# Kernel optimization log

Measured on AMD Instinct MI355X. Metric: run time of the kernel, lower is better.

The kernel has to match this reference:

```python
import jax, jax.numpy as jnp
import numpy as np

HIDDEN = 128


def setup_inputs() -> dict:
    key = jax.random.key(0)
    ks = jax.random.split(key, 9)
    N, D, OUT, DIM = 200000, 128, 128, 10000
    msg = jax.random.normal(ks[0], (N, D), dtype=jnp.float32)
    t = jax.random.uniform(ks[1], (N,), dtype=jnp.float32)
    index = jax.random.randint(ks[2], (N,), 0, DIM, dtype=jnp.int32)
    s = 1.0 / np.sqrt(HIDDEN)
    uni = lambda k, shape: jax.random.uniform(k, shape, jnp.float32, -s, s)
    return {
        "msg": msg,
        "t": t,
        "index": index,
        "dim_size": DIM,
        "W_ih": uni(ks[3], (3 * HIDDEN, D)),
        "W_hh": uni(ks[4], (3 * HIDDEN, HIDDEN)),
        "b_ih": uni(ks[5], (3 * HIDDEN,)),
        "b_hh": uni(ks[6], (3 * HIDDEN,)),
        "W_mlp": uni(ks[7], (OUT, HIDDEN)),
        "b_mlp": uni(ks[8], (OUT,)),
    }


def reference(msg, t, index, dim_size, W_ih, W_hh, b_ih, b_hh, W_mlp, b_mlp):
    # Sort messages by node id (primary) and timestamp (secondary). This matches
    # torch: sort by t, then group by index preserving time order within group.
    H = W_hh.shape[1]
    order = jnp.lexsort((t, index))
    idx_s = index[order]          # [N]
    msg_s = msg[order]            # [N, D]
    # segment starts: hidden state resets to 0 at the first message of each node
    start = jnp.concatenate([jnp.ones((1,), bool), idx_s[1:] != idx_s[:-1]])
    # precompute input-gate projections for all messages at once: [N, 3H]
    gi = msg_s @ W_ih.T + b_ih

    def step(h, inp):
        gi_t, st = inp
        h0 = jnp.where(st, jnp.zeros_like(h), h)
        gh = h0 @ W_hh.T + b_hh
        i_r, i_z, i_n = jnp.split(gi_t, 3)
        h_r, h_z, h_n = jnp.split(gh, 3)
        r = jax.nn.sigmoid(i_r + h_r)
        z = jax.nn.sigmoid(i_z + h_z)
        n = jnp.tanh(i_n + r * h_n)
        hn = (1.0 - z) * n + z * h0
        return hn, hn

    h0 = jnp.zeros((H,), msg.dtype)
    _, h_all = jax.lax.scan(step, h0, (gi, start))  # [N, H]

    # final hidden per node = hidden at last (latest-timestamp) message of that node
    pos = jnp.arange(idx_s.shape[0], dtype=jnp.int32)
    last_pos = jax.ops.segment_max(pos, idx_s, num_segments=dim_size)  # empty -> int32 min
    has_msg = last_pos >= 0
    h_node = h_all[jnp.clip(last_pos, 0, None)]     # [dim_size, H]
    out_vals = h_node @ W_mlp.T + b_mlp             # [dim_size, OUT]
    return jnp.where(has_msg[:, None], out_vals, jnp.zeros_like(out_vals))
```

## Files before the change

### kernel.cpp

```cpp
#include <hip/hip_runtime.h>
#include <hip/hip_fp16.h>

typedef _Float16 f16;
typedef _Float16 f16x8 __attribute__((ext_vector_type(8)));
typedef _Float16 f16x4 __attribute__((ext_vector_type(4)));
typedef float    f32x4 __attribute__((ext_vector_type(4)));
typedef unsigned long long u64;
typedef unsigned int u32;

#define HIDDEN 128
#define G3     384

__device__ inline float sigm(float x) { return 1.f / (1.f + __expf(-x)); }
__device__ inline float tanh_f(float x) {
  float ax = fabsf(x);
  float e  = __expf(2.f * ax);
  float r  = 1.f - 2.f / (e + 1.f);
  return x < 0.f ? -r : r;
}
__device__ inline f16x4 cvt4(float4 v) {
  return (f16x4){(f16)v.x, (f16)v.y, (f16)v.z, (f16)v.w};
}
__device__ inline f16x8 cvt8(float4 a, float4 b) {
  return (f16x8){(f16)a.x, (f16)a.y, (f16)a.z, (f16)a.w,
                 (f16)b.x, (f16)b.y, (f16)b.z, (f16)b.w};
}
__device__ inline f32x4 ld4(const float* p) { return *(const f32x4*)p; }


__global__ void hist_kernel(const int* __restrict__ idx, int* __restrict__ counts, int N) {
  int i = blockIdx.x * blockDim.x + threadIdx.x;
  if (i < N) atomicAdd(&counts[idx[i]], 1);
}

__global__ __launch_bounds__(1024) void meta_kernel(const int* __restrict__ counts,
                                                    int* __restrict__ offs,
                                                    int* __restrict__ order, int dim) {
  __shared__ int wsum[16], wpre[16];
  __shared__ int lhist[512], loffs[512], lcur[512];
  const int tid = threadIdx.x, lane = tid & 63, wid = tid >> 6;
  for (int i = tid; i < 512; i += 1024) { lhist[i] = 0; lcur[i] = 0; }
  __syncthreads();
  const int base_i = tid * 16;
  int loc[16];
  int s = 0;
#pragma unroll
  for (int u = 0; u < 16; u++) {
    int i = base_i + u;
    int x = (i < dim) ? counts[i] : 0;
    loc[u] = s; s += x;
    if (i < dim) atomicAdd(&lhist[511 - min(x, 511)], 1);
  }
  int inc = s;
#pragma unroll
  for (int d = 1; d < 64; d <<= 1) { int v = __shfl_up(inc, d, 64); if (lane >= d) inc += v; }
  if (lane == 63) wsum[wid] = inc;
  __syncthreads();
  if (wid == 0 && lane < 16) {
    int v = wsum[lane], p = v;
#pragma unroll
    for (int d = 1; d < 16; d <<= 1) { int q = __shfl_up(p, d, 16); if (lane >= d) p += q; }
    wpre[lane] = p - v;
  }
  __syncthreads();
  const int excl = wpre[wid] + inc - s;
#pragma unroll
  for (int u = 0; u < 16; u++) {
    int i = base_i + u;
    if (i < dim) offs[i] = excl + loc[u];
  }
  if (tid == 1023) offs[dim] = excl + s;
  __syncthreads();
  if (wid == 0) {
    int l8[8]; int ss = 0;
#pragma unroll
    for (int u = 0; u < 8; u++) { l8[u] = ss; ss += lhist[lane * 8 + u]; }
    int inc2 = ss;
#pragma unroll
    for (int d = 1; d < 64; d <<= 1) { int v = __shfl_up(inc2, d, 64); if (lane >= d) inc2 += v; }
    const int e2 = inc2 - ss;
#pragma unroll
    for (int u = 0; u < 8; u++) loffs[lane * 8 + u] = e2 + l8[u];
  }
  __syncthreads();
#pragma unroll
  for (int u = 0; u < 16; u++) {
    int g = base_i + u;
    if (g < dim) {
      int b = 511 - min(counts[g], 511);
      int p = loffs[b] + atomicAdd(&lcur[b], 1);
      order[p] = g;
    }
  }
}

__global__ void scatter_kernel(const float* __restrict__ t, const int* __restrict__ idx,
                               const int* __restrict__ off, int* __restrict__ cursor,
                               u64* __restrict__ keys, int* __restrict__ pos2g, int N) {
  int i = blockIdx.x * blockDim.x + threadIdx.x;
  if (i >= N) return;
  int g = idx[i];
  int p = off[g] + atomicAdd(&cursor[g], 1);
  keys[p] = ((u64)__float_as_uint(t[i]) << 32) | (u32)i;
  pos2g[p] = g;
}

__global__ void rank_kernel(const u64* __restrict__ keys, const int* __restrict__ pos2g,
                            const int* __restrict__ off, const int* __restrict__ cnt,
                            u64* __restrict__ keys2, int N) {
  int p = blockIdx.x * blockDim.x + threadIdx.x;
  if (p >= N) return;
  int g = pos2g[p];
  int s = off[g], m = cnt[g];
  u64 k = keys[p];
  int r = 0;
  for (int q = 0; q < m; q++) r += (keys[s + q] < k);
  keys2[s + r] = k;
}


__global__ __launch_bounds__(512) void recur4(
    const float* __restrict__ msg, const u64* __restrict__ keys,
    const int* __restrict__ off, const int* __restrict__ cnt,
    const float* __restrict__ W_ih, const float* __restrict__ W_hh,
    const float* __restrict__ b_ih, const float* __restrict__ b_hh,
    const float* __restrict__ W_mlp, const float* __restrict__ b_mlp,
    const int* __restrict__ order, float* __restrict__ out, int dim) {
  __shared__ __align__(16) f16 hB[2][16 * 128];
  __shared__ __align__(16) f16 mB[2][16 * 128];
  __shared__ int sArr[16], mArr[16];
  const int tid = threadIdx.x;
  const int q = tid >> 6, lane = tid & 63;
  const int c = lane & 15, hi = lane >> 4;
  const int ct = tid >> 5;
  const int j4 = (tid & 31) * 4;

  const int oidx = blockIdx.x * 16 + c;
  const bool valid = (oidx < dim);
  const int g = valid ? order[oidx] : 0;
  const int m = valid ? cnt[g] : 0;
  const int s = (valid && m > 0) ? off[g] : 0;
  if (tid < 16) { sArr[tid] = s; mArr[tid] = m; }
  int L = m;
#pragma unroll
  for (int d = 1; d < 16; d <<= 1) L = max(L, __shfl_xor(L, d, 16));

  f16x8 Ai[3][4], Ah[3][4];
#pragma unroll
  for (int p = 0; p < 3; p++)
#pragma unroll
    for (int kt = 0; kt < 4; kt++) {
      const size_t ro = (size_t)(p * 128 + q * 16 + c) * 128 + kt * 32 + hi * 8;
      Ai[p][kt] = cvt8(*(const float4*)(W_ih + ro), *(const float4*)(W_ih + ro + 4));
      Ah[p][kt] = cvt8(*(const float4*)(W_hh + ro), *(const float4*)(W_hh + ro + 4));
    }
  const int rb = q * 16 + hi * 4;
  const f32x4 bR  = ld4(b_ih + rb)       + ld4(b_hh + rb);
  const f32x4 bZ  = ld4(b_ih + 128 + rb) + ld4(b_hh + 128 + rb);
  const f32x4 bNi = ld4(b_ih + 256 + rb);
  const f32x4 bNh = ld4(b_hh + 256 + rb);

  float h0[4] = {0.f, 0.f, 0.f, 0.f};
  *(f16x4*)&hB[0][c * 128 + ((q ^ (c & 7)) * 16) + hi * 4] =
      (f16x4){(f16)0.f, (f16)0.f, (f16)0.f, (f16)0.f};
  __syncthreads();

  const u32* keysLo = (const u32*)keys;
  const int sc = sArr[ct], mc = mArr[ct];
  {
    const u32 mid0 = keysLo[2 * sc];
    const float4 v = *(const float4*)(msg + (size_t)mid0 * 128 + j4);
    const int tk = j4 >> 4;
    *(f16x4*)&mB[0][ct * 128 + ((tk ^ (ct & 7)) * 16) + (j4 & 15)] = cvt4(v);
  }
  __syncthreads();

  for (int st = 0; st < L; ++st) {
    const f16* hr = hB[st & 1];
    const f16* mr = mB[st & 1];
    f16x8 Bh[4], Bm[4];
#pragma unroll
    for (int kt = 0; kt < 4; kt++) {
      const int ad = c * 128 + (((2 * kt + (hi >> 1)) ^ (c & 7)) * 16) + (hi & 1) * 8;
      Bh[kt] = *(const f16x8*)&hr[ad];
      Bm[kt] = *(const f16x8*)&mr[ad];
    }
    const bool stg = (st + 1 < L);
    float4 v;
    if (stg) {
      const int pos = sc + max(0, min(st + 1, mc - 1));
      const u32 midn = keysLo[2 * pos];
      v = *(const float4*)(msg + (size_t)midn * 128 + j4);
    }
    f32x4 Cr = bR, Cz = bZ, Cni = bNi, Cnh = bNh;
#pragma unroll
    for (int kt = 0; kt < 4; kt++) Cr  = __builtin_amdgcn_mfma_f32_16x16x32_f16(Ai[0][kt], Bm[kt], Cr, 0, 0, 0);
#pragma unroll
    for (int kt = 0; kt < 4; kt++) Cr  = __builtin_amdgcn_mfma_f32_16x16x32_f16(Ah[0][kt], Bh[kt], Cr, 0, 0, 0);
#pragma unroll
    for (int kt = 0; kt < 4; kt++) Cz  = __builtin_amdgcn_mfma_f32_16x16x32_f16(Ai[1][kt], Bm[kt], Cz, 0, 0, 0);
#pragma unroll
    for (int kt = 0; kt < 4; kt++) Cz  = __builtin_amdgcn_mfma_f32_16x16x32_f16(Ah[1][kt], Bh[kt], Cz, 0, 0, 0);
#pragma unroll
    for (int kt = 0; kt < 4; kt++) Cni = __builtin_amdgcn_mfma_f32_16x16x32_f16(Ai[2][kt], Bm[kt], Cni, 0, 0, 0);
#pragma unroll
    for (int kt = 0; kt < 4; kt++) Cnh = __builtin_amdgcn_mfma_f32_16x16x32_f16(Ah[2][kt], Bh[kt], Cnh, 0, 0, 0);
    const bool act = (st < m);
#pragma unroll
    for (int qq = 0; qq < 4; qq++) {
      float r = sigm(Cr[qq]);
      float z = sigm(Cz[qq]);
      float n = tanh_f(Cni[qq] + r * Cnh[qq]);
      if (act) h0[qq] = (1.f - z) * n + z * h0[qq];
    }
    *(f16x4*)&hB[(st + 1) & 1][c * 128 + ((q ^ (c & 7)) * 16) + hi * 4] =
        (f16x4){(f16)h0[0], (f16)h0[1], (f16)h0[2], (f16)h0[3]};
    if (stg) {
      const int tk = j4 >> 4;
      *(f16x4*)&mB[(st + 1) & 1][ct * 128 + ((tk ^ (ct & 7)) * 16) + (j4 & 15)] = cvt4(v);
    }
    __syncthreads();
  }

  const f16* hf = hB[L & 1];
  f16x8 Bf[4];
#pragma unroll
  for (int kt = 0; kt < 4; kt++) {
    const int ad = c * 128 + (((2 * kt + (hi >> 1)) ^ (c & 7)) * 16) + (hi & 1) * 8;
    Bf[kt] = *(const f16x8*)&hf[ad];
  }
  f32x4 o = ld4(b_mlp + q * 16 + hi * 4);
#pragma unroll
  for (int kt = 0; kt < 4; kt++) {
    const size_t wo = (size_t)(q * 16 + c) * 128 + kt * 32 + hi * 8;
    f16x8 Af = cvt8(*(const float4*)(W_mlp + wo), *(const float4*)(W_mlp + wo + 4));
    o = __builtin_amdgcn_mfma_f32_16x16x32_f16(Af, Bf[kt], o, 0, 0, 0);
  }
  if (valid) {
    const f32x4 oz = (m > 0) ? o : (f32x4){0.f, 0.f, 0.f, 0.f};
    *(f32x4*)(out + (size_t)g * 128 + q * 16 + hi * 4) = oz;
  }
}


extern "C" void kernel_launch(void* const* d_in, const int* in_sizes, int n_in,
                              void* d_out, int out_size, void* d_ws, size_t ws_size,
                              hipStream_t stream) {
  const float* msg   = (const float*)d_in[0];
  const float* t     = (const float*)d_in[1];
  const int*   indx  = (const int*)d_in[2];
  const float* W_ih  = (const float*)d_in[4];
  const float* W_hh  = (const float*)d_in[5];
  const float* b_ih  = (const float*)d_in[6];
  const float* b_hh  = (const float*)d_in[7];
  const float* W_mlp = (const float*)d_in[8];
  const float* b_mlp = (const float*)d_in[9];
  float* out = (float*)d_out;
  const int N   = in_sizes[0] / 128;
  const int dim = out_size / 128;
  const int nb  = (dim + 15) / 16;

  char* ws = (char*)d_ws;
  size_t o = 0;
  auto alloc = [&](size_t b) { size_t r = o; o = (o + b + 255) & ~(size_t)255; return r; };
  u64* keys   = (u64*)(ws + alloc((size_t)N * 8));
  u64* keys2  = (u64*)(ws + alloc((size_t)N * 8));
  int* pos2g  = (int*)(ws + alloc((size_t)N * 4));
  int* offs   = (int*)(ws + alloc((size_t)(dim + 1) * 4));
  int* order  = (int*)(ws + alloc((size_t)dim * 4));
  size_t meta_bytes = (size_t)(2 * dim) * 4;
  char* meta  = ws + alloc(meta_bytes);
  int* counts = (int*)meta;
  int* cursor = (int*)(meta + (size_t)dim * 4);

  hipMemsetAsync(meta, 0, meta_bytes, stream);

  const int gN = (N + 255) / 256;
  hist_kernel<<<gN, 256, 0, stream>>>(indx, counts, N);
  meta_kernel<<<1, 1024, 0, stream>>>(counts, offs, order, dim);
  scatter_kernel<<<gN, 256, 0, stream>>>(t, indx, offs, cursor, keys, pos2g, N);
  rank_kernel<<<gN, 256, 0, stream>>>(keys, pos2g, offs, counts, keys2, N);

  recur4<<<nb, 512, 0, stream>>>(msg, keys2, offs, counts, W_ih, W_hh, b_ih, b_hh,
                                 W_mlp, b_mlp, order, out, dim);
}
```

Before: 350.1 us.

## Use persistent blocks with atomic work queue and deeper key prefetch in GRU recurrence

Replaces the one-block-per-16-node launch with a persistent grid of up to 512 blocks that pull node batches from a global atomic counter. The weight fragments are loaded into registers once per block instead of once per batch. The message key index is now prefetched two steps ahead to shorten the dependent load chain, and launch bounds request 4 blocks per CU. This trades an extra atomic and barriers per batch, plus register pressure from the occupancy hint, for less weight reloading and better load balance across batches of uneven length.

New measurement: 438.5 us. +25.3%, slower.

```diff
diff --git a/kernel.cpp b/kernel.cpp
--- a/kernel.cpp
+++ b/kernel.cpp
@@ -119,32 +119,24 @@
 }
 
 
-__global__ __launch_bounds__(512) void recur4(
+__global__ __launch_bounds__(512, 4) void recur5(
     const float* __restrict__ msg, const u64* __restrict__ keys,
     const int* __restrict__ off, const int* __restrict__ cnt,
     const float* __restrict__ W_ih, const float* __restrict__ W_hh,
     const float* __restrict__ b_ih, const float* __restrict__ b_hh,
     const float* __restrict__ W_mlp, const float* __restrict__ b_mlp,
-    const int* __restrict__ order, float* __restrict__ out, int dim) {
+    const int* __restrict__ order, float* __restrict__ out,
+    int dim, int nbatch, int* __restrict__ qctr) {
   __shared__ __align__(16) f16 hB[2][16 * 128];
   __shared__ __align__(16) f16 mB[2][16 * 128];
   __shared__ int sArr[16], mArr[16];
+  __shared__ int nextb;
   const int tid = threadIdx.x;
   const int q = tid >> 6, lane = tid & 63;
   const int c = lane & 15, hi = lane >> 4;
   const int ct = tid >> 5;
   const int j4 = (tid & 31) * 4;
 
-  const int oidx = blockIdx.x * 16 + c;
-  const bool valid = (oidx < dim);
-  const int g = valid ? order[oidx] : 0;
-  const int m = valid ? cnt[g] : 0;
-  const int s = (valid && m > 0) ? off[g] : 0;
-  if (tid < 16) { sArr[tid] = s; mArr[tid] = m; }
-  int L = m;
-#pragma unroll
-  for (int d = 1; d < 16; d <<= 1) L = max(L, __shfl_xor(L, d, 16));
-
   f16x8 Ai[3][4], Ah[3][4];
 #pragma unroll
   for (int p = 0; p < 3; p++)
@@ -159,86 +151,105 @@
   const f32x4 bZ  = ld4(b_ih + 128 + rb) + ld4(b_hh + 128 + rb);
   const f32x4 bNi = ld4(b_ih + 256 + rb);
   const f32x4 bNh = ld4(b_hh + 256 + rb);
-
-  float h0[4] = {0.f, 0.f, 0.f, 0.f};
-  *(f16x4*)&hB[0][c * 128 + ((q ^ (c & 7)) * 16) + hi * 4] =
-      (f16x4){(f16)0.f, (f16)0.f, (f16)0.f, (f16)0.f};
-  __syncthreads();
-
   const u32* keysLo = (const u32*)keys;
-  const int sc = sArr[ct], mc = mArr[ct];
-  {
-    const u32 mid0 = keysLo[2 * sc];
-    const float4 v = *(const float4*)(msg + (size_t)mid0 * 128 + j4);
-    const int tk = j4 >> 4;
-    *(f16x4*)&mB[0][ct * 128 + ((tk ^ (ct & 7)) * 16) + (j4 & 15)] = cvt4(v);
-  }
-  __syncthreads();
-
-  for (int st = 0; st < L; ++st) {
-    const f16* hr = hB[st & 1];
-    const f16* mr = mB[st & 1];
-    f16x8 Bh[4], Bm[4];
+
+  while (true) {
+    if (tid == 0) nextb = atomicAdd(qctr, 1);
+    __syncthreads();
+    const int b = nextb;
+    __syncthreads();
+    if (b >= nbatch) break;
+
+    const int oidx = b * 16 + c;
+    const bool valid = (oidx < dim);
+    const int g = valid ? order[oidx] : 0;
+    const int m = valid ? cnt[g] : 0;
+    const int s = (valid && m > 0) ? off[g] : 0;
+    if (tid < 16) { sArr[tid] = s; mArr[tid] = m; }
+    int L = m;
+#pragma unroll
+    for (int d = 1; d < 16; d <<= 1) L = max(L, __shfl_xor(L, d, 16));
+
+    float h0[4] = {0.f, 0.f, 0.f, 0.f};
+    *(f16x4*)&hB[0][c * 128 + ((q ^ (c & 7)) * 16) + hi * 4] =
+        (f16x4){(f16)0.f, (f16)0.f, (f16)0.f, (f16)0.f};
+    __syncthreads();
+
+    const int sc = sArr[ct], mc = mArr[ct];
+    {
+      const u32 mid0 = keysLo[2 * sc];
+      const float4 v = *(const float4*)(msg + (size_t)mid0 * 128 + j4);
+      const int tk = j4 >> 4;
+      *(f16x4*)&mB[0][ct * 128 + ((tk ^ (ct & 7)) * 16) + (j4 & 15)] = cvt4(v);
+    }
+    u32 kNext = keysLo[2 * (sc + max(0, min(1, mc - 1)))];
+    __syncthreads();
+
+    for (int st = 0; st < L; ++st) {
+      const bool stg = (st + 1 < L);
+      float4 v;
+      if (stg) v = *(const float4*)(msg + (size_t)kNext * 128 + j4);
+      u32 kNext2 = kNext;
+      if (st + 2 < L) kNext2 = keysLo[2 * (sc + max(0, min(st + 2, mc - 1)))];
+
+      const f16* hr = hB[st & 1];
+      const f16* mr = mB[st & 1];
+      f16x8 Bh[4], Bm[4];
+#pragma unroll
+      for (int kt = 0; kt < 4; kt++) {
+        const int ad = c * 128 + (((2 * kt + (hi >> 1)) ^ (c & 7)) * 16) + (hi & 1) * 8;
+        Bh[kt] = *(const f16x8*)&hr[ad];
+        Bm[kt] = *(const f16x8*)&mr[ad];
+      }
+      f32x4 Cr = bR, Cz = bZ, Cni = bNi, Cnh = bNh;
+#pragma unroll
+      for (int kt = 0; kt < 4; kt++) Cr  = __builtin_amdgcn_mfma_f32_16x16x32_f16(Ai[0][kt], Bm[kt], Cr, 0, 0, 0);
+#pragma unroll
+      for (int kt = 0; kt < 4; kt++) Cr  = __builtin_amdgcn_mfma_f32_16x16x32_f16(Ah[0][kt], Bh[kt], Cr, 0, 0, 0);
+#pragma unroll
+      for (int kt = 0; kt < 4; kt++) Cz  = __builtin_amdgcn_mfma_f32_16x16x32_f16(Ai[1][kt], Bm[kt], Cz, 0, 0, 0);
+#pragma unroll
+      for (int kt = 0; kt < 4; kt++) Cz  = __builtin_amdgcn_mfma_f32_16x16x32_f16(Ah[1][kt], Bh[kt], Cz, 0, 0, 0);
+#pragma unroll
+      for (int kt = 0; kt < 4; kt++) Cni = __builtin_amdgcn_mfma_f32_16x16x32_f16(Ai[2][kt], Bm[kt], Cni, 0, 0, 0);
+#pragma unroll
+      for (int kt = 0; kt < 4; kt++) Cnh = __builtin_amdgcn_mfma_f32_16x16x32_f16(Ah[2][kt], Bh[kt], Cnh, 0, 0, 0);
+      const bool act = (st < m);
+#pragma unroll
+      for (int qq = 0; qq < 4; qq++) {
+        float r = sigm(Cr[qq]);
+        float z = sigm(Cz[qq]);
+        float n = tanh_f(Cni[qq] + r * Cnh[qq]);
+        if (act) h0[qq] = (1.f - z) * n + z * h0[qq];
+      }
+      *(f16x4*)&hB[(st + 1) & 1][c * 128 + ((q ^ (c & 7)) * 16) + hi * 4] =
+          (f16x4){(f16)h0[0], (f16)h0[1], (f16)h0[2], (f16)h0[3]};
+      if (stg) {
+        const int tk = j4 >> 4;
+        *(f16x4*)&mB[(st + 1) & 1][ct * 128 + ((tk ^ (ct & 7)) * 16) + (j4 & 15)] = cvt4(v);
+      }
+      __syncthreads();
+      kNext = kNext2;
+    }
+
+    const f16* hf = hB[L & 1];
+    f16x8 Bf[4];
 #pragma unroll
     for (int kt = 0; kt < 4; kt++) {
       const int ad = c * 128 + (((2 * kt + (hi >> 1)) ^ (c & 7)) * 16) + (hi & 1) * 8;
-      Bh[kt] = *(const f16x8*)&hr[ad];
-      Bm[kt] = *(const f16x8*)&mr[ad];
-    }
-    const bool stg = (st + 1 < L);
-    float4 v;
-    if (stg) {
-      const int pos = sc + max(0, min(st + 1, mc - 1));
-      const u32 midn = keysLo[2 * pos];
-      v = *(const float4*)(msg + (size_t)midn * 128 + j4);
-    }
-    f32x4 Cr = bR, Cz = bZ, Cni = bNi, Cnh = bNh;
-#pragma unroll
-    for (int kt = 0; kt < 4; kt++) Cr  = __builtin_amdgcn_mfma_f32_16x16x32_f16(Ai[0][kt], Bm[kt], Cr, 0, 0, 0);
-#pragma unroll
-    for (int kt = 0; kt < 4; kt++) Cr  = __builtin_amdgcn_mfma_f32_16x16x32_f16(Ah[0][kt], Bh[kt], Cr, 0, 0, 0);
-#pragma unroll
-    for (int kt = 0; kt < 4; kt++) Cz  = __builtin_amdgcn_mfma_f32_16x16x32_f16(Ai[1][kt], Bm[kt], Cz, 0, 0, 0);
-#pragma unroll
-    for (int kt = 0; kt < 4; kt++) Cz  = __builtin_amdgcn_mfma_f32_16x16x32_f16(Ah[1][kt], Bh[kt], Cz, 0, 0, 0);
-#pragma unroll
-    for (int kt = 0; kt < 4; kt++) Cni = __builtin_amdgcn_mfma_f32_16x16x32_f16(Ai[2][kt], Bm[kt], Cni, 0, 0, 0);
-#pragma unroll
-    for (int kt = 0; kt < 4; kt++) Cnh = __builtin_amdgcn_mfma_f32_16x16x32_f16(Ah[2][kt], Bh[kt], Cnh, 0, 0, 0);
-    const bool act = (st < m);
-#pragma unroll
-    for (int qq = 0; qq < 4; qq++) {
-      float r = sigm(Cr[qq]);
-      float z = sigm(Cz[qq]);
-      float n = tanh_f(Cni[qq] + r * Cnh[qq]);
-      if (act) h0[qq] = (1.f - z) * n + z * h0[qq];
-    }
-    *(f16x4*)&hB[(st + 1) & 1][c * 128 + ((q ^ (c & 7)) * 16) + hi * 4] =
-        (f16x4){(f16)h0[0], (f16)h0[1], (f16)h0[2], (f16)h0[3]};
-    if (stg) {
-      const int tk = j4 >> 4;
-      *(f16x4*)&mB[(st + 1) & 1][ct * 128 + ((tk ^ (ct & 7)) * 16) + (j4 & 15)] = cvt4(v);
-    }
-    __syncthreads();
-  }
-
-  const f16* hf = hB[L & 1];
-  f16x8 Bf[4];
-#pragma unroll
-  for (int kt = 0; kt < 4; kt++) {
-    const int ad = c * 128 + (((2 * kt + (hi >> 1)) ^ (c & 7)) * 16) + (hi & 1) * 8;
-    Bf[kt] = *(const f16x8*)&hf[ad];
-  }
-  f32x4 o = ld4(b_mlp + q * 16 + hi * 4);
-#pragma unroll
-  for (int kt = 0; kt < 4; kt++) {
-    const size_t wo = (size_t)(q * 16 + c) * 128 + kt * 32 + hi * 8;
-    f16x8 Af = cvt8(*(const float4*)(W_mlp + wo), *(const float4*)(W_mlp + wo + 4));
-    o = __builtin_amdgcn_mfma_f32_16x16x32_f16(Af, Bf[kt], o, 0, 0, 0);
-  }
-  if (valid) {
-    const f32x4 oz = (m > 0) ? o : (f32x4){0.f, 0.f, 0.f, 0.f};
-    *(f32x4*)(out + (size_t)g * 128 + q * 16 + hi * 4) = oz;
+      Bf[kt] = *(const f16x8*)&hf[ad];
+    }
+    f32x4 o = ld4(b_mlp + q * 16 + hi * 4);
+#pragma unroll
+    for (int kt = 0; kt < 4; kt++) {
+      const size_t wo = (size_t)(q * 16 + c) * 128 + kt * 32 + hi * 8;
+      f16x8 Af = cvt8(*(const float4*)(W_mlp + wo), *(const float4*)(W_mlp + wo + 4));
+      o = __builtin_amdgcn_mfma_f32_16x16x32_f16(Af, Bf[kt], o, 0, 0, 0);
+    }
+    if (valid) {
+      const f32x4 oz = (m > 0) ? o : (f32x4){0.f, 0.f, 0.f, 0.f};
+      *(f32x4*)(out + (size_t)g * 128 + q * 16 + hi * 4) = oz;
+    }
   }
 }
 
@@ -268,10 +279,11 @@
   int* pos2g  = (int*)(ws + alloc((size_t)N * 4));
   int* offs   = (int*)(ws + alloc((size_t)(dim + 1) * 4));
   int* order  = (int*)(ws + alloc((size_t)dim * 4));
-  size_t meta_bytes = (size_t)(2 * dim) * 4;
+  size_t meta_bytes = (size_t)(2 * dim + 64) * 4;
   char* meta  = ws + alloc(meta_bytes);
   int* counts = (int*)meta;
   int* cursor = (int*)(meta + (size_t)dim * 4);
+  int* qctr   = (int*)(meta + (size_t)2 * dim * 4);
 
   hipMemsetAsync(meta, 0, meta_bytes, stream);
 
@@ -281,6 +293,7 @@
   scatter_kernel<<<gN, 256, 0, stream>>>(t, indx, offs, cursor, keys, pos2g, N);
   rank_kernel<<<gN, 256, 0, stream>>>(keys, pos2g, offs, counts, keys2, N);
 
-  recur4<<<nb, 512, 0, stream>>>(msg, keys2, offs, counts, W_ih, W_hh, b_ih, b_hh,
-                                 W_mlp, b_mlp, order, out, dim);
-}
+  const int pgrid = min(512, nb);
+  recur5<<<pgrid, 512, 0, stream>>>(msg, keys2, offs, counts, W_ih, W_hh, b_ih, b_hh,
+                                    W_mlp, b_mlp, order, out, dim, nb, qctr);
+}
```
